# Kernel tuning notes

Hardware: AMD Instinct MI355X
Metric: run time of the kernel (lower is better)

The kernel has to match this reference:

```python
import jax, jax.numpy as jnp
import numpy as np

DIM = 768
HEADS = 12
DIM_HEAD = 64
INNER = HEADS * DIM_HEAD  # 768
SCALE = DIM_HEAD ** -0.5


def setup_inputs() -> dict:
    key = jax.random.key(0)
    k1, k2, k3, k4 = jax.random.split(key, 4)
    b, n = 8, 1024
    x = jax.random.normal(k1, (b, n, DIM), dtype=jnp.float32)
    # fused QKV projection, no bias: y = x @ w_qkv  -> [b, n, 3*inner]
    w_qkv = jax.random.normal(k2, (DIM, 3 * INNER), dtype=jnp.float32) * (DIM ** -0.5)
    # output projection with bias
    w_out = jax.random.normal(k3, (INNER, DIM), dtype=jnp.float32) * (INNER ** -0.5)
    b_out = jax.random.normal(k4, (DIM,), dtype=jnp.float32) * 0.02
    return {"x": x, "w_qkv": w_qkv, "w_out": w_out, "b_out": b_out}


def reference(x, w_qkv, w_out, b_out):
    b, n, _ = x.shape
    qkv = jnp.einsum('bnd,de->bne', x, w_qkv)  # [b, n, 3*inner]
    q, k, v = jnp.split(qkv, 3, axis=-1)
    # 'b n (h d) -> b h n d'
    def split_heads(t):
        return t.reshape(b, n, HEADS, DIM_HEAD).transpose(0, 2, 1, 3)
    q, k, v = split_heads(q), split_heads(k), split_heads(v)
    dots = jnp.einsum('bhid,bhjd->bhij', q, k) * SCALE  # [b, h, n, n]
    attn = jax.nn.softmax(dots, axis=-1)
    out = jnp.einsum('bhij,bhjd->bhid', attn, v)  # [b, h, n, d]
    out = out.transpose(0, 2, 1, 3).reshape(b, n, INNER)  # 'b h n d -> b n (h d)'
    return jnp.einsum('bne,ed->bnd', out, w_out) + b_out
```

## Files before the change

kernel.cpp:

```cpp
#include <hip/hip_runtime.h>

typedef unsigned short u16;
typedef __bf16 bf16x8 __attribute__((ext_vector_type(8)));
typedef float f32x4 __attribute__((ext_vector_type(4)));

__device__ inline u16 f2bf(float f) {
    union { float f; unsigned int u; } a; a.f = f;
    unsigned int u = a.u + 0x7fffu + ((a.u >> 16) & 1u);
    return (u16)(u >> 16);
}

__device__ __forceinline__ void cp16(const void* g, void* l) {
    __builtin_amdgcn_global_load_lds(
        (const __attribute__((address_space(1))) unsigned int*)g,
        (__attribute__((address_space(3))) unsigned int*)l, 16, 0, 0);
}

__global__ __launch_bounds__(256) void prep(
    const float* __restrict__ x, const float* __restrict__ wq,
    const float* __restrict__ wo, u16* __restrict__ xbf,
    u16* __restrict__ wtq, u16* __restrict__ wto)
{
    int bid = blockIdx.x;
    if (bid < 3072) {
        size_t base = ((size_t)bid * 256 + threadIdx.x) * 8;
        float4 f0 = *(const float4*)&x[base];
        float4 f1 = *(const float4*)&x[base + 4];
        union { u16 s[8]; uint4 v; } t;
        t.s[0]=f2bf(f0.x); t.s[1]=f2bf(f0.y); t.s[2]=f2bf(f0.z); t.s[3]=f2bf(f0.w);
        t.s[4]=f2bf(f1.x); t.s[5]=f2bf(f1.y); t.s[6]=f2bf(f1.z); t.s[7]=f2bf(f1.w);
        *(uint4*)&xbf[base] = t.v;
        return;
    }
    __shared__ u16 tile[32][33];
    const float* in; u16* outp; int N, bx, by;
    if (bid < 3072 + 1728) { int t = bid - 3072; in = wq; outp = wtq; N = 2304; bx = t % 72; by = t / 72; }
    else                   { int t = bid - 4800; in = wo; outp = wto; N = 768;  bx = t % 24; by = t / 24; }
    int n0 = bx * 32, k0 = by * 32;
    int tx = threadIdx.x & 31, ty = threadIdx.x >> 5;
    #pragma unroll
    for (int r = ty; r < 32; r += 8)
        tile[r][tx] = f2bf(in[(size_t)(k0 + r) * N + n0 + tx]);
    __syncthreads();
    #pragma unroll
    for (int r = ty; r < 32; r += 8)
        outp[(size_t)(n0 + r) * 768 + k0 + tx] = tile[tx][r];
}

__global__ __launch_bounds__(256) void gemm_qkv(
    const u16* __restrict__ A, const u16* __restrict__ Bt,
    u16* __restrict__ q_out, u16* __restrict__ k_out, u16* __restrict__ v_out)
{
    const int K = 768;
    __shared__ __align__(16) u16 As[2][128 * 64];
    __shared__ __align__(16) u16 Bs[2][128 * 64];

    int tid = threadIdx.x;
    int lane = tid & 63, wave = tid >> 6;
    int quad = lane >> 4, l16 = lane & 15;
    int wm = wave >> 1, wn = wave & 1;
    int id = blockIdx.x;
    int xcd = id & 7, j = id >> 3;
    int m0 = (((j & 7) << 3) + xcd) * 128;
    int n0 = (j >> 3) * 128;

    f32x4 acc[4][4];
    #pragma unroll
    for (int i = 0; i < 4; i++)
        #pragma unroll
        for (int jj = 0; jj < 4; jj++) acc[i][jj] = (f32x4){0.f, 0.f, 0.f, 0.f};

    int r0 = tid >> 3, cg = tid & 7;
    int g = cg ^ (r0 & 7);
    const u16* GA[4]; const u16* GB[4];
    #pragma unroll
    for (int it = 0; it < 4; it++) {
        GA[it] = A  + (size_t)(m0 + it * 32 + r0) * K + g * 8;
        GB[it] = Bt + (size_t)(n0 + it * 32 + r0) * K + g * 8;
    }

    #define STAGE_QKV(kt, b)                                          \
        _Pragma("unroll")                                             \
        for (int it = 0; it < 4; it++) {                              \
            cp16(GA[it] + (kt), &As[b][(it * 256 + tid) * 8]);        \
            cp16(GB[it] + (kt), &Bs[b][(it * 256 + tid) * 8]);        \
        }

    STAGE_QKV(0, 0)
    for (int i = 0; i < 12; i++) {
        int b = i & 1;
        if (i + 1 < 12) {
            STAGE_QKV((i + 1) * 64, b ^ 1)
            asm volatile("s_waitcnt vmcnt(8)" ::: "memory");
        } else {
            asm volatile("s_waitcnt vmcnt(0)" ::: "memory");
        }
        __builtin_amdgcn_s_barrier();
        bf16x8 af[2][4], bfr[2][4];
        #pragma unroll
        for (int ko = 0; ko < 2; ko++)
            #pragma unroll
            for (int x = 0; x < 4; x++) {
                int Ra = wm * 64 + x * 16 + l16;
                af[ko][x]  = *(const bf16x8*)&As[b][Ra * 64 + (((ko * 4 + quad) ^ (Ra & 7)) * 8)];
                int Rb = wn * 64 + x * 16 + l16;
                bfr[ko][x] = *(const bf16x8*)&Bs[b][Rb * 64 + (((ko * 4 + quad) ^ (Rb & 7)) * 8)];
            }
        #pragma unroll
        for (int ko = 0; ko < 2; ko++)
            #pragma unroll
            for (int x = 0; x < 4; x++)
                #pragma unroll
                for (int y = 0; y < 4; y++)
                    acc[x][y] = __builtin_amdgcn_mfma_f32_16x16x32_bf16(af[ko][x], bfr[ko][y], acc[x][y], 0, 0, 0);
        __builtin_amdgcn_s_barrier();
    }
    #undef STAGE_QKV

    int M0 = m0 + wm * 64, N0 = n0 + wn * 64;
    int part = N0 >= 1536 ? 2 : (N0 >= 768 ? 1 : 0);
    int h = (N0 - part * 768) >> 6;
    int b2 = M0 >> 10, npos0 = M0 & 1023;
    u16* ep = (wave < 2 ? As[0] : Bs[0]) + (wave & 1) * 4096;

    if (part != 2) {
        float scale = (part == 0) ? 0.18033688011112042f : 1.0f;
        u16* gbase = (part == 0 ? q_out : k_out) + (((size_t)(b2 * 12 + h) * 1024 + npos0) << 6);
        #pragma unroll
        for (int i = 0; i < 4; i++)
            #pragma unroll
            for (int jj = 0; jj < 4; jj++) {
                int dd = jj * 16 + l16;
                #pragma unroll
                for (int r = 0; r < 4; r++) {
                    int np = i * 16 + quad * 4 + r;
                    ep[np * 64 + (((dd >> 3) ^ (np & 7)) * 8) + (dd & 7)] =
                        f2bf(acc[i][jj][r] * scale);
                }
            }
        #pragma unroll
        for (int t = 0; t < 8; t++) {
            int idx = t * 512 + lane * 8;
            int np = idx >> 6;
            int slot = ((lane & 7) ^ (np & 7));
            uint4 v = *(const uint4*)&ep[np * 64 + slot * 8];
            *(uint4*)&gbase[idx] = v;
        }
    } else {
        #pragma unroll
        for (int i = 0; i < 4; i++)
            #pragma unroll
            for (int jj = 0; jj < 4; jj++) {
                int dd = jj * 16 + l16;
                int npg = i * 2 + (quad >> 1);
                int sub = (quad & 1) * 4;
                union { u16 s[4]; uint2 v; } pk;
                #pragma unroll
                for (int r = 0; r < 4; r++) pk.s[r] = f2bf(acc[i][jj][r]);
                *(uint2*)&ep[dd * 64 + ((npg ^ (dd & 7)) * 8) + sub] = pk.v;
            }
        #pragma unroll
        for (int t = 0; t < 8; t++) {
            int dd = t * 8 + (lane >> 3);
            int npg = lane & 7;
            uint4 v = *(const uint4*)&ep[dd * 64 + ((npg ^ (dd & 7)) * 8)];
            *(uint4*)&v_out[((size_t)((b2 * 12 + h) * 64 + dd)) * 1024 + npos0 + npg * 8] = v;
        }
    }
}

__global__ __launch_bounds__(256) void attn128(
    u16* __restrict__ QO, const u16* __restrict__ Kg, const u16* __restrict__ Vtg)
{
    __shared__ __align__(16) u16 Ks[2][64 * 64];
    __shared__ __align__(16) u16 Vs[2][64 * 64];

    int tid = threadIdx.x;
    int lane = tid & 63, wave = tid >> 6;
    int quad = lane >> 4, l16 = lane & 15;
    int id = blockIdx.x;
    int xcd = id & 7, j = id >> 3;
    int bh = xcd * 12 + (j >> 3);
    int q0 = (j & 7) * 128;
    const size_t head_base = (size_t)bh * 65536;

    size_t qoff[2];
    bf16x8 qf[2][2];
    #pragma unroll
    for (int qs = 0; qs < 2; qs++) {
        qoff[qs] = head_base + (size_t)(q0 + wave * 32 + qs * 16 + l16) * 64;
        qf[qs][0] = *(const bf16x8*)&QO[qoff[qs] + quad * 8];
        qf[qs][1] = *(const bf16x8*)&QO[qoff[qs] + 32 + quad * 8];
    }

    f32x4 Oacc[4][2];
    #pragma unroll
    for (int dt = 0; dt < 4; dt++)
        #pragma unroll
        for (int qs = 0; qs < 2; qs++) Oacc[dt][qs] = (f32x4){0.f, 0.f, 0.f, 0.f};
    f32x4 lacc[2];
    lacc[0] = (f32x4){0.f, 0.f, 0.f, 0.f};
    lacc[1] = (f32x4){0.f, 0.f, 0.f, 0.f};

    union { unsigned int w[4]; bf16x8 v; } ones;
    ones.w[0] = ones.w[1] = ones.w[2] = ones.w[3] = 0x3f803f80u;

    int srow = tid >> 3, sg = tid & 7;
    int gsK = sg ^ (srow & 7);
    const u16* GK[2];
    GK[0] = Kg + head_base + (size_t)(srow) * 64 + gsK * 8;
    GK[1] = Kg + head_base + (size_t)(32 + srow) * 64 + gsK * 8;
    const u16* GV[2];
    GV[0] = Vtg + head_base + (size_t)(srow) * 1024 + sg * 8;
    GV[1] = Vtg + head_base + (size_t)(32 + srow) * 1024 + sg * 8;
    int vwA[2], vwB[2];
    #pragma unroll
    for (int it = 0; it < 2; it++) {
        int r = it * 32 + srow;
        vwA[it] = r * 64 + (((2 * sg)     ^ (r & 15)) * 4);
        vwB[it] = r * 64 + (((2 * sg + 1) ^ (r & 15)) * 4);
    }

    uint4 vA0, vA1, vB0, vB1;

    {
        uint4 t0 = *(const uint4*)GV[0];
        uint4 t1 = *(const uint4*)GV[1];
        uint2 t;
        t.x = t0.x; t.y = t0.y; *(uint2*)&Vs[0][vwA[0]] = t;
        t.x = t0.z; t.y = t0.w; *(uint2*)&Vs[0][vwB[0]] = t;
        t.x = t1.x; t.y = t1.y; *(uint2*)&Vs[0][vwA[1]] = t;
        t.x = t1.z; t.y = t1.w; *(uint2*)&Vs[0][vwB[1]] = t;
    }
    vA0 = *(const uint4*)(GV[0] + 64);
    vA1 = *(const uint4*)(GV[1] + 64);
    cp16(GK[0], &Ks[0][(0 * 256 + tid) * 8]);
    cp16(GK[1], &Ks[0][(1 * 256 + tid) * 8]);
    asm volatile("s_waitcnt lgkmcnt(0)" ::: "memory");

    #define ATT_PF(I, PFV, PFK, VN0, VN1)                                        \
        if (PFV) {                                                               \
            VN0 = *(const uint4*)(GV[0] + ((I) + 2) * 64);                       \
            VN1 = *(const uint4*)(GV[1] + ((I) + 2) * 64);                       \
        }                                                                        \
        if (PFK) {                                                               \
            cp16(GK[0] + (size_t)((I) + 1) * 4096, &Ks[((I) + 1) & 1][(0 * 256 + tid) * 8]); \
            cp16(GK[1] + (size_t)((I) + 1) * 4096, &Ks[((I) + 1) & 1][(1 * 256 + tid) * 8]); \
        }

    #define ATT_COMP(I, WRV, VC0, VC1)                                           \
    {                                                                            \
        int b = (I) & 1;                                                         \
        __builtin_amdgcn_s_barrier();                                            \
        bf16x8 kf[4][2];                                                         \
        _Pragma("unroll")                                                        \
        for (int nt = 0; nt < 4; nt++) {                                         \
            int R = nt * 16 + l16;                                               \
            kf[nt][0] = *(const bf16x8*)&Ks[b][R * 64 + ((quad       ^ (R & 7)) * 8)]; \
            kf[nt][1] = *(const bf16x8*)&Ks[b][R * 64 + (((quad + 4) ^ (R & 7)) * 8)]; \
        }                                                                        \
        if (WRV) {                                                               \
            uint2 t;                                                             \
            t.x = VC0.x; t.y = VC0.y; *(uint2*)&Vs[b ^ 1][vwA[0]] = t;           \
            t.x = VC0.z; t.y = VC0.w; *(uint2*)&Vs[b ^ 1][vwB[0]] = t;           \
            t.x = VC1.x; t.y = VC1.y; *(uint2*)&Vs[b ^ 1][vwA[1]] = t;           \
            t.x = VC1.z; t.y = VC1.w; *(uint2*)&Vs[b ^ 1][vwB[1]] = t;           \
        }                                                                        \
        f32x4 s4[4][2];                                                          \
        _Pragma("unroll")                                                        \
        for (int nt = 0; nt < 4; nt++)                                           \
            _Pragma("unroll")                                                    \
            for (int qs = 0; qs < 2; qs++) {                                     \
                f32x4 s = (f32x4){0.f, 0.f, 0.f, 0.f};                           \
                s = __builtin_amdgcn_mfma_f32_16x16x32_bf16(kf[nt][0], qf[qs][0], s, 0, 0, 0); \
                s = __builtin_amdgcn_mfma_f32_16x16x32_bf16(kf[nt][1], qf[qs][1], s, 0, 0, 0); \
                s4[nt][qs] = s;                                                  \
            }                                                                    \
        float p[4][2][4];                                                        \
        _Pragma("unroll")                                                        \
        for (int nt = 0; nt < 4; nt++)                                           \
            _Pragma("unroll")                                                    \
            for (int qs = 0; qs < 2; qs++)                                       \
                _Pragma("unroll")                                                \
                for (int r = 0; r < 4; r++)                                      \
                    p[nt][qs][r] = __builtin_amdgcn_exp2f(s4[nt][qs][r]);        \
        __builtin_amdgcn_s_setprio(1);                                           \
        _Pragma("unroll")                                                        \
        for (int h = 0; h < 2; h++) {                                            \
            union { unsigned int w[4]; bf16x8 v; } pk[2];                        \
            _Pragma("unroll")                                                    \
            for (int qs = 0; qs < 2; qs++) {                                     \
                asm("v_cvt_pk_bf16_f32 %0, %1, %2" : "=v"(pk[qs].w[0]) : "v"(p[2*h][qs][0]),   "v"(p[2*h][qs][1])); \
                asm("v_cvt_pk_bf16_f32 %0, %1, %2" : "=v"(pk[qs].w[1]) : "v"(p[2*h][qs][2]),   "v"(p[2*h][qs][3])); \
                asm("v_cvt_pk_bf16_f32 %0, %1, %2" : "=v"(pk[qs].w[2]) : "v"(p[2*h+1][qs][0]), "v"(p[2*h+1][qs][1])); \
                asm("v_cvt_pk_bf16_f32 %0, %1, %2" : "=v"(pk[qs].w[3]) : "v"(p[2*h+1][qs][2]), "v"(p[2*h+1][qs][3])); \
                lacc[qs] = __builtin_amdgcn_mfma_f32_16x16x32_bf16(ones.v, pk[qs].v, lacc[qs], 0, 0, 0); \
            }                                                                    \
            int pbase = ((8 * h + quad) ^ l16) * 4;                              \
            _Pragma("unroll")                                                    \
            for (int dt = 0; dt < 4; dt++) {                                     \
                int drow = dt * 16 + l16;                                        \
                union { u16 s[8]; bf16x8 v; } vk;                                \
                *(uint2*)&vk.s[0] = *(const uint2*)&Vs[b][drow * 64 + pbase];    \
                *(uint2*)&vk.s[4] = *(const uint2*)&Vs[b][drow * 64 + (pbase ^ 16)]; \
                _Pragma("unroll")                                                \
                for (int qs = 0; qs < 2; qs++)                                   \
                    Oacc[dt][qs] = __builtin_amdgcn_mfma_f32_16x16x32_bf16(vk.v, pk[qs].v, Oacc[dt][qs], 0, 0, 0); \
            }                                                                    \
        }                                                                        \
        __builtin_amdgcn_s_setprio(0);                                           \
        asm volatile("s_waitcnt lgkmcnt(0)" ::: "memory");                       \
        __builtin_amdgcn_s_barrier();                                            \
    }

    for (int ii = 0; ii < 7; ii++) {
        int i0 = 2 * ii, i1 = i0 + 1;
        ATT_PF(i0, 1, 1, vB0, vB1)
        asm volatile("s_waitcnt vmcnt(4)" ::: "memory");
        ATT_COMP(i0, 1, vA0, vA1)
        ATT_PF(i1, 1, 1, vA0, vA1)
        asm volatile("s_waitcnt vmcnt(4)" ::: "memory");
        ATT_COMP(i1, 1, vB0, vB1)
    }
    ATT_PF(14, 0, 1, vB0, vB1)
    asm volatile("s_waitcnt vmcnt(2)" ::: "memory");
    ATT_COMP(14, 1, vA0, vA1)
    asm volatile("s_waitcnt vmcnt(0)" ::: "memory");
    ATT_COMP(15, 0, vB0, vB1)

    #undef ATT_PF
    #undef ATT_COMP

    #pragma unroll
    for (int qs = 0; qs < 2; qs++) {
        float rl = __builtin_amdgcn_rcpf(lacc[qs][0]);
        #pragma unroll
        for (int dt = 0; dt < 4; dt++) {
            union { u16 s[4]; uint2 v; } ok;
            #pragma unroll
            for (int r = 0; r < 4; r++) ok.s[r] = f2bf(Oacc[dt][qs][r] * rl);
            *(uint2*)&QO[qoff[qs] + dt * 16 + quad * 4] = ok.v;
        }
    }
}

__global__ __launch_bounds__(256) void gemm_out(
    const u16* __restrict__ Qg, const u16* __restrict__ Bt,
    const float* __restrict__ bias, float* __restrict__ out)
{
    const int K = 768;
    __shared__ __align__(16) u16 As[2][128 * 64];
    __shared__ __align__(16) u16 Bs[2][128 * 64];

    int tid = threadIdx.x;
    int lane = tid & 63, wave = tid >> 6;
    int quad = lane >> 4, l16 = lane & 15;
    int wm = wave >> 1, wn = wave & 1;
    int id = blockIdx.x;
    int xcd = id & 7, j = id >> 3;
    int m0 = (((j & 7) << 3) + xcd) * 128;
    int n0 = (j >> 3) * 128;

    f32x4 acc[4][4];
    #pragma unroll
    for (int i = 0; i < 4; i++)
        #pragma unroll
        for (int jj = 0; jj < 4; jj++) acc[i][jj] = (f32x4){0.f, 0.f, 0.f, 0.f};

    int r0 = tid >> 3, cg = tid & 7;
    int g = cg ^ (r0 & 7);
    const u16* GA[4]; const u16* GB[4];
    #pragma unroll
    for (int it = 0; it < 4; it++) {
        int m = m0 + it * 32 + r0, b = m >> 10, npos = m & 1023;
        GA[it] = Qg + (((size_t)(b * 12) * 1024 + npos) << 6) + g * 8;
        GB[it] = Bt + (size_t)(n0 + it * 32 + r0) * K + g * 8;
    }

    #define STAGE_OUT(i2, b)                                              \
        _Pragma("unroll")                                                 \
        for (int it = 0; it < 4; it++) {                                  \
            cp16(GA[it] + (size_t)(i2) * 65536, &As[b][(it * 256 + tid) * 8]); \
            cp16(GB[it] + (i2) * 64,            &Bs[b][(it * 256 + tid) * 8]); \
        }

    STAGE_OUT(0, 0)
    for (int i = 0; i < 12; i++) {
        int b = i & 1;
        if (i + 1 < 12) {
            STAGE_OUT(i + 1, b ^ 1)
            asm volatile("s_waitcnt vmcnt(8)" ::: "memory");
        } else {
            asm volatile("s_waitcnt vmcnt(0)" ::: "memory");
        }
        __builtin_amdgcn_s_barrier();
        bf16x8 af[2][4], bfr[2][4];
        #pragma unroll
        for (int ko = 0; ko < 2; ko++)
            #pragma unroll
            for (int x = 0; x < 4; x++) {
                int Ra = wm * 64 + x * 16 + l16;
                af[ko][x]  = *(const bf16x8*)&As[b][Ra * 64 + (((ko * 4 + quad) ^ (Ra & 7)) * 8)];
                int Rb = wn * 64 + x * 16 + l16;
                bfr[ko][x] = *(const bf16x8*)&Bs[b][Rb * 64 + (((ko * 4 + quad) ^ (Rb & 7)) * 8)];
            }
        #pragma unroll
        for (int ko = 0; ko < 2; ko++)
            #pragma unroll
            for (int x = 0; x < 4; x++)
                #pragma unroll
                for (int y = 0; y < 4; y++)
                    acc[x][y] = __builtin_amdgcn_mfma_f32_16x16x32_bf16(af[ko][x], bfr[ko][y], acc[x][y], 0, 0, 0);
        __builtin_amdgcn_s_barrier();
    }
    #undef STAGE_OUT

    #pragma unroll
    for (int i = 0; i < 4; i++) {
        int mbase = m0 + wm * 64 + i * 16 + quad * 4;
        #pragma unroll
        for (int jj = 0; jj < 4; jj++) {
            int n = n0 + wn * 64 + jj * 16 + l16;
            float bv = bias[n];
            #pragma unroll
            for (int r = 0; r < 4; r++)
                out[(size_t)(mbase + r) * 768 + n] = acc[i][jj][r] + bv;
        }
    }
}

extern "C" void kernel_launch(void* const* d_in, const int* in_sizes, int n_in,
                              void* d_out, int out_size, void* d_ws, size_t ws_size,
                              hipStream_t stream) {
    const float* x     = (const float*)d_in[0];
    const float* w_qkv = (const float*)d_in[1];
    const float* w_out = (const float*)d_in[2];
    const float* b_out = (const float*)d_in[3];
    float* out = (float*)d_out;

    char* ws = (char*)d_ws;
    u16* wtq  = (u16*)(ws);
    u16* wto  = (u16*)(ws + 3538944);
    u16* Qbuf = (u16*)(ws + 4718592);
    u16* xbf  = (u16*)(ws + 17301504);
    u16* Kbuf = (u16*)d_out;
    u16* Vbuf = (u16*)d_out + 6291456;

    prep<<<dim3(5376), 256, 0, stream>>>(x, w_qkv, w_out, xbf, wtq, wto);
    gemm_qkv<<<dim3(1152), 256, 0, stream>>>(xbf, wtq, Qbuf, Kbuf, Vbuf);
    attn128<<<dim3(768), 256, 0, stream>>>(Qbuf, Kbuf, Vbuf);
    gemm_out<<<dim3(384), 256, 0, stream>>>(Qbuf, wto, b_out, out);
}
```

Before: 187.7 us.

## Split attention block across 8 waves with 16 query rows each

The attention kernel now launches 512 threads per block, so eight waves each own 16 query rows instead of four waves owning 32. Every thread loads one K and one V chunk per tile instead of two. The per-wave register footprint roughly halves, and launch bounds request higher occupancy. The prefetch schedule is simplified to a full vmcnt/lgkmcnt wait plus a single barrier per step, which may expose more memory latency in exchange for more waves to hide it.

Result: faster. 179.8 us (-4.2%).

```diff
diff --git a/kernel.cpp b/kernel.cpp
--- a/kernel.cpp
+++ b/kernel.cpp
@@ -169,7 +169,7 @@
     }
 }
 
-__global__ __launch_bounds__(256) void attn128(
+__global__ __launch_bounds__(512, 6) void attn128(
     u16* __restrict__ QO, const u16* __restrict__ Kg, const u16* __restrict__ Vtg)
 {
     __shared__ __align__(16) u16 Ks[2][64 * 64];
@@ -184,118 +184,74 @@
     int q0 = (j & 7) * 128;
     const size_t head_base = (size_t)bh * 65536;
 
-    size_t qoff[2];
-    bf16x8 qf[2][2];
-    #pragma unroll
-    for (int qs = 0; qs < 2; qs++) {
-        qoff[qs] = head_base + (size_t)(q0 + wave * 32 + qs * 16 + l16) * 64;
-        qf[qs][0] = *(const bf16x8*)&QO[qoff[qs] + quad * 8];
-        qf[qs][1] = *(const bf16x8*)&QO[qoff[qs] + 32 + quad * 8];
-    }
-
-    f32x4 Oacc[4][2];
-    #pragma unroll
-    for (int dt = 0; dt < 4; dt++)
-        #pragma unroll
-        for (int qs = 0; qs < 2; qs++) Oacc[dt][qs] = (f32x4){0.f, 0.f, 0.f, 0.f};
-    f32x4 lacc[2];
-    lacc[0] = (f32x4){0.f, 0.f, 0.f, 0.f};
-    lacc[1] = (f32x4){0.f, 0.f, 0.f, 0.f};
+    size_t qoff = head_base + (size_t)(q0 + wave * 16 + l16) * 64;
+    bf16x8 qf0 = *(const bf16x8*)&QO[qoff + quad * 8];
+    bf16x8 qf1 = *(const bf16x8*)&QO[qoff + 32 + quad * 8];
+
+    f32x4 Oacc[4];
+    #pragma unroll
+    for (int dt = 0; dt < 4; dt++) Oacc[dt] = (f32x4){0.f, 0.f, 0.f, 0.f};
+    f32x4 lacc = (f32x4){0.f, 0.f, 0.f, 0.f};
 
     union { unsigned int w[4]; bf16x8 v; } ones;
     ones.w[0] = ones.w[1] = ones.w[2] = ones.w[3] = 0x3f803f80u;
 
     int srow = tid >> 3, sg = tid & 7;
     int gsK = sg ^ (srow & 7);
-    const u16* GK[2];
-    GK[0] = Kg + head_base + (size_t)(srow) * 64 + gsK * 8;
-    GK[1] = Kg + head_base + (size_t)(32 + srow) * 64 + gsK * 8;
-    const u16* GV[2];
-    GV[0] = Vtg + head_base + (size_t)(srow) * 1024 + sg * 8;
-    GV[1] = Vtg + head_base + (size_t)(32 + srow) * 1024 + sg * 8;
-    int vwA[2], vwB[2];
-    #pragma unroll
-    for (int it = 0; it < 2; it++) {
-        int r = it * 32 + srow;
-        vwA[it] = r * 64 + (((2 * sg)     ^ (r & 15)) * 4);
-        vwB[it] = r * 64 + (((2 * sg + 1) ^ (r & 15)) * 4);
-    }
-
-    uint4 vA0, vA1, vB0, vB1;
-
+    const u16* GK = Kg + head_base + (size_t)srow * 64 + gsK * 8;
+    const u16* GV = Vtg + head_base + (size_t)srow * 1024 + sg * 8;
+    const int vwA = srow * 64 + (((2 * sg)     ^ (srow & 15)) * 4);
+    const int vwB = srow * 64 + (((2 * sg + 1) ^ (srow & 15)) * 4);
+
+    uint4 vA, vB;
     {
-        uint4 t0 = *(const uint4*)GV[0];
-        uint4 t1 = *(const uint4*)GV[1];
+        uint4 t0 = *(const uint4*)GV;
         uint2 t;
-        t.x = t0.x; t.y = t0.y; *(uint2*)&Vs[0][vwA[0]] = t;
-        t.x = t0.z; t.y = t0.w; *(uint2*)&Vs[0][vwB[0]] = t;
-        t.x = t1.x; t.y = t1.y; *(uint2*)&Vs[0][vwA[1]] = t;
-        t.x = t1.z; t.y = t1.w; *(uint2*)&Vs[0][vwB[1]] = t;
-    }
-    vA0 = *(const uint4*)(GV[0] + 64);
-    vA1 = *(const uint4*)(GV[1] + 64);
-    cp16(GK[0], &Ks[0][(0 * 256 + tid) * 8]);
-    cp16(GK[1], &Ks[0][(1 * 256 + tid) * 8]);
-    asm volatile("s_waitcnt lgkmcnt(0)" ::: "memory");
-
-    #define ATT_PF(I, PFV, PFK, VN0, VN1)                                        \
-        if (PFV) {                                                               \
-            VN0 = *(const uint4*)(GV[0] + ((I) + 2) * 64);                       \
-            VN1 = *(const uint4*)(GV[1] + ((I) + 2) * 64);                       \
+        t.x = t0.x; t.y = t0.y; *(uint2*)&Vs[0][vwA] = t;
+        t.x = t0.z; t.y = t0.w; *(uint2*)&Vs[0][vwB] = t;
+    }
+    vA = *(const uint4*)(GV + 64);
+    cp16(GK, &Ks[0][tid * 8]);
+
+    #define ATT_STEP(I, DO_K, DO_LD, VLD, DO_WR, VWR)                            \
+    {                                                                            \
+        const int b = (I) & 1;                                                   \
+        asm volatile("s_waitcnt vmcnt(0)" ::: "memory");                         \
+        asm volatile("s_waitcnt lgkmcnt(0)" ::: "memory");                       \
+        __builtin_amdgcn_s_barrier();                                            \
+        if (DO_K) cp16(GK + (size_t)((I) + 1) * 4096, &Ks[b ^ 1][tid * 8]);      \
+        if (DO_LD) VLD = *(const uint4*)(GV + ((I) + 2) * 64);                   \
+        if (DO_WR) {                                                             \
+            uint2 t;                                                             \
+            t.x = VWR.x; t.y = VWR.y; *(uint2*)&Vs[b ^ 1][vwA] = t;              \
+            t.x = VWR.z; t.y = VWR.w; *(uint2*)&Vs[b ^ 1][vwB] = t;              \
         }                                                                        \
-        if (PFK) {                                                               \
-            cp16(GK[0] + (size_t)((I) + 1) * 4096, &Ks[((I) + 1) & 1][(0 * 256 + tid) * 8]); \
-            cp16(GK[1] + (size_t)((I) + 1) * 4096, &Ks[((I) + 1) & 1][(1 * 256 + tid) * 8]); \
-        }
-
-    #define ATT_COMP(I, WRV, VC0, VC1)                                           \
-    {                                                                            \
-        int b = (I) & 1;                                                         \
-        __builtin_amdgcn_s_barrier();                                            \
-        bf16x8 kf[4][2];                                                         \
+        f32x4 s4[4];                                                             \
         _Pragma("unroll")                                                        \
         for (int nt = 0; nt < 4; nt++) {                                         \
             int R = nt * 16 + l16;                                               \
-            kf[nt][0] = *(const bf16x8*)&Ks[b][R * 64 + ((quad       ^ (R & 7)) * 8)]; \
-            kf[nt][1] = *(const bf16x8*)&Ks[b][R * 64 + (((quad + 4) ^ (R & 7)) * 8)]; \
+            bf16x8 kf0 = *(const bf16x8*)&Ks[b][R * 64 + ((quad       ^ (R & 7)) * 8)]; \
+            bf16x8 kf1 = *(const bf16x8*)&Ks[b][R * 64 + (((quad + 4) ^ (R & 7)) * 8)]; \
+            f32x4 s = (f32x4){0.f, 0.f, 0.f, 0.f};                               \
+            s = __builtin_amdgcn_mfma_f32_16x16x32_bf16(kf0, qf0, s, 0, 0, 0);   \
+            s = __builtin_amdgcn_mfma_f32_16x16x32_bf16(kf1, qf1, s, 0, 0, 0);   \
+            s4[nt] = s;                                                          \
         }                                                                        \
-        if (WRV) {                                                               \
-            uint2 t;                                                             \
-            t.x = VC0.x; t.y = VC0.y; *(uint2*)&Vs[b ^ 1][vwA[0]] = t;           \
-            t.x = VC0.z; t.y = VC0.w; *(uint2*)&Vs[b ^ 1][vwB[0]] = t;           \
-            t.x = VC1.x; t.y = VC1.y; *(uint2*)&Vs[b ^ 1][vwA[1]] = t;           \
-            t.x = VC1.z; t.y = VC1.w; *(uint2*)&Vs[b ^ 1][vwB[1]] = t;           \
-        }                                                                        \
-        f32x4 s4[4][2];                                                          \
+        float p[4][4];                                                           \
         _Pragma("unroll")                                                        \
         for (int nt = 0; nt < 4; nt++)                                           \
             _Pragma("unroll")                                                    \
-            for (int qs = 0; qs < 2; qs++) {                                     \
-                f32x4 s = (f32x4){0.f, 0.f, 0.f, 0.f};                           \
-                s = __builtin_amdgcn_mfma_f32_16x16x32_bf16(kf[nt][0], qf[qs][0], s, 0, 0, 0); \
-                s = __builtin_amdgcn_mfma_f32_16x16x32_bf16(kf[nt][1], qf[qs][1], s, 0, 0, 0); \
-                s4[nt][qs] = s;                                                  \
-            }                                                                    \
-        float p[4][2][4];                                                        \
-        _Pragma("unroll")                                                        \
-        for (int nt = 0; nt < 4; nt++)                                           \
-            _Pragma("unroll")                                                    \
-            for (int qs = 0; qs < 2; qs++)                                       \
-                _Pragma("unroll")                                                \
-                for (int r = 0; r < 4; r++)                                      \
-                    p[nt][qs][r] = __builtin_amdgcn_exp2f(s4[nt][qs][r]);        \
+            for (int r = 0; r < 4; r++)                                          \
+                p[nt][r] = __builtin_amdgcn_exp2f(s4[nt][r]);                    \
         __builtin_amdgcn_s_setprio(1);                                           \
         _Pragma("unroll")                                                        \
         for (int h = 0; h < 2; h++) {                                            \
-            union { unsigned int w[4]; bf16x8 v; } pk[2];                        \
-            _Pragma("unroll")                                                    \
-            for (int qs = 0; qs < 2; qs++) {                                     \
-                asm("v_cvt_pk_bf16_f32 %0, %1, %2" : "=v"(pk[qs].w[0]) : "v"(p[2*h][qs][0]),   "v"(p[2*h][qs][1])); \
-                asm("v_cvt_pk_bf16_f32 %0, %1, %2" : "=v"(pk[qs].w[1]) : "v"(p[2*h][qs][2]),   "v"(p[2*h][qs][3])); \
-                asm("v_cvt_pk_bf16_f32 %0, %1, %2" : "=v"(pk[qs].w[2]) : "v"(p[2*h+1][qs][0]), "v"(p[2*h+1][qs][1])); \
-                asm("v_cvt_pk_bf16_f32 %0, %1, %2" : "=v"(pk[qs].w[3]) : "v"(p[2*h+1][qs][2]), "v"(p[2*h+1][qs][3])); \
-                lacc[qs] = __builtin_amdgcn_mfma_f32_16x16x32_bf16(ones.v, pk[qs].v, lacc[qs], 0, 0, 0); \
-            }                                                                    \
+            union { unsigned int w[4]; bf16x8 v; } pk;                           \
+            asm("v_cvt_pk_bf16_f32 %0, %1, %2" : "=v"(pk.w[0]) : "v"(p[2*h][0]),   "v"(p[2*h][1]));   \
+            asm("v_cvt_pk_bf16_f32 %0, %1, %2" : "=v"(pk.w[1]) : "v"(p[2*h][2]),   "v"(p[2*h][3]));   \
+            asm("v_cvt_pk_bf16_f32 %0, %1, %2" : "=v"(pk.w[2]) : "v"(p[2*h+1][0]), "v"(p[2*h+1][1])); \
+            asm("v_cvt_pk_bf16_f32 %0, %1, %2" : "=v"(pk.w[3]) : "v"(p[2*h+1][2]), "v"(p[2*h+1][3])); \
+            lacc = __builtin_amdgcn_mfma_f32_16x16x32_bf16(ones.v, pk.v, lacc, 0, 0, 0); \
             int pbase = ((8 * h + quad) ^ l16) * 4;                              \
             _Pragma("unroll")                                                    \
             for (int dt = 0; dt < 4; dt++) {                                     \
@@ -303,43 +259,28 @@
                 union { u16 s[8]; bf16x8 v; } vk;                                \
                 *(uint2*)&vk.s[0] = *(const uint2*)&Vs[b][drow * 64 + pbase];    \
                 *(uint2*)&vk.s[4] = *(const uint2*)&Vs[b][drow * 64 + (pbase ^ 16)]; \
-                _Pragma("unroll")                                                \
-                for (int qs = 0; qs < 2; qs++)                                   \
-                    Oacc[dt][qs] = __builtin_amdgcn_mfma_f32_16x16x32_bf16(vk.v, pk[qs].v, Oacc[dt][qs], 0, 0, 0); \
+                Oacc[dt] = __builtin_amdgcn_mfma_f32_16x16x32_bf16(vk.v, pk.v, Oacc[dt], 0, 0, 0); \
             }                                                                    \
         }                                                                        \
         __builtin_amdgcn_s_setprio(0);                                           \
-        asm volatile("s_waitcnt lgkmcnt(0)" ::: "memory");                       \
-        __builtin_amdgcn_s_barrier();                                            \
     }
 
     for (int ii = 0; ii < 7; ii++) {
-        int i0 = 2 * ii, i1 = i0 + 1;
-        ATT_PF(i0, 1, 1, vB0, vB1)
-        asm volatile("s_waitcnt vmcnt(4)" ::: "memory");
-        ATT_COMP(i0, 1, vA0, vA1)
-        ATT_PF(i1, 1, 1, vA0, vA1)
-        asm volatile("s_waitcnt vmcnt(4)" ::: "memory");
-        ATT_COMP(i1, 1, vB0, vB1)
-    }
-    ATT_PF(14, 0, 1, vB0, vB1)
-    asm volatile("s_waitcnt vmcnt(2)" ::: "memory");
-    ATT_COMP(14, 1, vA0, vA1)
-    asm volatile("s_waitcnt vmcnt(0)" ::: "memory");
-    ATT_COMP(15, 0, vB0, vB1)
-
-    #undef ATT_PF
-    #undef ATT_COMP
-
-    #pragma unroll
-    for (int qs = 0; qs < 2; qs++) {
-        float rl = __builtin_amdgcn_rcpf(lacc[qs][0]);
+        ATT_STEP(2 * ii,     1, 1, vB, 1, vA)
+        ATT_STEP(2 * ii + 1, 1, 1, vA, 1, vB)
+    }
+    ATT_STEP(14, 1, 0, vB, 1, vA)
+    ATT_STEP(15, 0, 0, vA, 0, vB)
+    #undef ATT_STEP
+
+    {
+        float rl = __builtin_amdgcn_rcpf(lacc[0]);
         #pragma unroll
         for (int dt = 0; dt < 4; dt++) {
             union { u16 s[4]; uint2 v; } ok;
             #pragma unroll
-            for (int r = 0; r < 4; r++) ok.s[r] = f2bf(Oacc[dt][qs][r] * rl);
-            *(uint2*)&QO[qoff[qs] + dt * 16 + quad * 4] = ok.v;
+            for (int r = 0; r < 4; r++) ok.s[r] = f2bf(Oacc[dt][r] * rl);
+            *(uint2*)&QO[qoff + dt * 16 + quad * 4] = ok.v;
         }
     }
 }
@@ -448,6 +389,6 @@
 
     prep<<<dim3(5376), 256, 0, stream>>>(x, w_qkv, w_out, xbf, wtq, wto);
     gemm_qkv<<<dim3(1152), 256, 0, stream>>>(xbf, wtq, Qbuf, Kbuf, Vbuf);
-    attn128<<<dim3(768), 256, 0, stream>>>(Qbuf, Kbuf, Vbuf);
+    attn128<<<dim3(768), 512, 0, stream>>>(Qbuf, Kbuf, Vbuf);
     gemm_out<<<dim3(384), 256, 0, stream>>>(Qbuf, wto, b_out, out);
 }
```
